# Optimization experiments

Hardware: AMD Instinct MI355X
Metric: run time of the kernel (lower is better)

## Reference

```python
import jax, jax.numpy as jnp
import numpy as np

RULE_START = 85
N_RULE = 20
N_OUTPUT = 33
N_RNN = 1024
T, B = 256, 256
ALPHA = 0.2
SIGMA = 0.05


def setup_inputs() -> dict:
    key = jax.random.key(0)
    ks = jax.random.split(key, 9)
    x = jax.random.normal(ks[0], (T, B, RULE_START + N_RULE), dtype=jnp.float32)
    # torch.rand_like -> uniform [0,1), scaled by sigma_rec (precomputed for all steps)
    noise = jax.random.uniform(ks[1], (T, B, N_RNN), dtype=jnp.float32) * SIGMA
    s = 0.05  # small init scale to keep softplus in a sane range
    W_sens = jax.random.normal(ks[2], (N_RNN, RULE_START), dtype=jnp.float32) * s
    b_sens = jax.random.normal(ks[3], (N_RNN,), dtype=jnp.float32) * s
    W_rule = jax.random.normal(ks[4], (N_RNN, N_RULE), dtype=jnp.float32) * s
    W_rec = jax.random.normal(ks[5], (N_RNN, N_RNN), dtype=jnp.float32) * s
    b_rec = jax.random.normal(ks[6], (N_RNN,), dtype=jnp.float32) * s
    W_out = jax.random.normal(ks[7], (N_OUTPUT, N_RNN), dtype=jnp.float32) * s
    b_out = jax.random.normal(ks[8], (N_OUTPUT,), dtype=jnp.float32) * s
    return {"x": x, "noise": noise, "W_sens": W_sens, "b_sens": b_sens,
            "W_rule": W_rule, "W_rec": W_rec, "b_rec": b_rec,
            "W_out": W_out, "b_out": b_out}


def reference(x, noise, W_sens, b_sens, W_rule, W_rec, b_rec, W_out, b_out):
    # x: [T, B, rule_start + n_rule]
    sensory = x[:, :, :RULE_START]
    rule = x[:, :, RULE_START:]
    # input projections applied once for all timesteps: [T, B, H]
    rnn_inputs = (jnp.einsum('tbi,hi->tbh', sensory, W_sens) + b_sens
                  + jnp.einsum('tbr,hr->tbh', rule, W_rule))

    h0 = jnp.zeros_like(rnn_inputs[0])  # [B, H]

    def step(h, inp_nz):
        inp, nz = inp_nz
        out = jax.nn.softplus(inp + nz + h @ W_rec.T + b_rec)
        h = ALPHA * out + (1.0 - ALPHA) * h
        return h, h

    _, hidden_states = jax.lax.scan(step, h0, (rnn_inputs, noise))  # [T, B, H]
    return jnp.einsum('tbh,oh->tbo', hidden_states, W_out) + b_out
```

## Files before the change

### kernel.cpp

```cpp
#include <hip/hip_runtime.h>
#include <cstdint>
#include <cstddef>

#define TSTEPS 256
#define NB     256
#define NH     1024
#define NIN    105
#define NOUT   33
#define NGRP   8
#define NSL    16

using half8 = __attribute__((ext_vector_type(8))) _Float16;
using f32x4 = __attribute__((ext_vector_type(4))) float;


__global__ __launch_bounds__(256) void k_convert(
    const float* __restrict__ W_sens, const float* __restrict__ W_rule,
    const float* __restrict__ W_rec,  const float* __restrict__ W_out,
    _Float16* __restrict__ Wrecf, _Float16* __restrict__ Wcf,
    _Float16* __restrict__ Wof)
{
    int tid  = blockIdx.x * 256 + threadIdx.x;
    int lane = tid & 63;
    int orow = lane & 15;
    int col0 = (lane >> 4) * 8;
    if (tid < 64 * 32 * 64) {
        int kk = (tid >> 6) & 31, n = tid >> 11;
        int o = n * 16 + orow, k0 = kk * 32 + col0;
        const float* s = W_rec + (size_t)o * NH + k0;
        _Float16* d = Wrecf + (size_t)tid * 8;
        #pragma unroll
        for (int j = 0; j < 8; ++j) d[j] = (_Float16)s[j];
    } else if (tid < 64 * 32 * 64 + 64 * 4 * 64) {
        int t2 = tid - 64 * 32 * 64;
        int kk = (t2 >> 6) & 3, n = t2 >> 8;
        int o = n * 16 + orow, k0 = kk * 32 + col0;
        _Float16* d = Wcf + (size_t)t2 * 8;
        #pragma unroll
        for (int j = 0; j < 8; ++j) {
            int k = k0 + j;
            float v = 0.f;
            if (k < 85)       v = W_sens[o * 85 + k];
            else if (k < NIN) v = W_rule[o * 20 + (k - 85)];
            d[j] = (_Float16)v;
        }
    } else {
        int t3 = tid - (64 * 32 * 64 + 64 * 4 * 64);
        int kk = (t3 >> 6) & 31, n = t3 >> 11;
        int o = n * 16 + orow, k0 = kk * 32 + col0;
        _Float16* d = Wof + (size_t)t3 * 8;
        #pragma unroll
        for (int j = 0; j < 8; ++j)
            d[j] = (o < NOUT) ? (_Float16)W_out[(size_t)o * NH + k0 + j]
                              : (_Float16)0.f;
    }
}

__global__ __launch_bounds__(256) void k_init(uint32_t* __restrict__ hGw,
                                              uint32_t* __restrict__ flags)
{
    int tid = blockIdx.x * 256 + threadIdx.x;
    if (tid < 262144) hGw[tid] = 0u;
    if (tid < 256)    flags[tid] = 0u;
}

#define XS_STRIDE 136
__global__ __launch_bounds__(256) void k_ingemm(
    const float* __restrict__ x, float* __restrict__ pre,
    const float* __restrict__ b_sens, const float* __restrict__ b_rec,
    const _Float16* __restrict__ Wcf)
{
    __shared__ _Float16 xs[64 * XS_STRIDE];
    int tid = threadIdx.x;
    int bm  = blockIdx.x;
    int nc  = blockIdx.y;
    const float* xsrc = x + (size_t)bm * 64 * NIN;
    for (int idx = tid; idx < 64 * NIN; idx += 256) {
        int r = idx / NIN, c = idx - r * NIN;
        xs[r * XS_STRIDE + c] = (_Float16)xsrc[idx];
    }
    for (int idx = tid; idx < 64 * (XS_STRIDE - NIN); idx += 256) {
        int r = idx / (XS_STRIDE - NIN);
        int c = NIN + (idx - r * (XS_STRIDE - NIN));
        xs[r * XS_STRIDE + c] = (_Float16)0.f;
    }
    __syncthreads();

    int wave = tid >> 6, lane = tid & 63;
    int mrow = lane & 15, q = lane >> 4;
    f32x4 acc[16];
    #pragma unroll
    for (int nt = 0; nt < 16; ++nt) acc[nt] = (f32x4){0.f, 0.f, 0.f, 0.f};
    const half8* Wc8 = (const half8*)Wcf;

    #pragma unroll
    for (int kk = 0; kk < 4; ++kk) {
        half8 a = *(const half8*)&xs[(wave * 16 + mrow) * XS_STRIDE + kk * 32 + q * 8];
        #pragma unroll
        for (int nt = 0; nt < 16; ++nt) {
            int ng = nc * 16 + nt;
            half8 b = Wc8[(ng * 4 + kk) * 64 + lane];
            acc[nt] = __builtin_amdgcn_mfma_f32_16x16x32_f16(a, b, acc[nt], 0, 0, 0);
        }
    }
    #pragma unroll
    for (int nt = 0; nt < 16; ++nt) {
        int o = nc * 256 + nt * 16 + mrow;
        float bias = b_sens[o] + b_rec[o];
        #pragma unroll
        for (int r = 0; r < 4; ++r) {
            size_t R = (size_t)bm * 64 + wave * 16 + q * 4 + r;
            size_t ad = R * NH + o;
            pre[ad] = acc[nt][r] + bias + pre[ad];
        }
    }
}

__global__ __launch_bounds__(512, 1) void k_rnn(
    float* __restrict__ pre, const _Float16* __restrict__ Wrecf,
    _Float16* __restrict__ hG, int* __restrict__ arr, int* __restrict__ xcdArr)
{
    __shared__ _Float16 Wl[4 * 32 * 64 * 8];
    __shared__ float red[8][64][4];
    __shared__ int sFast;

    const int tid  = threadIdx.x;
    const int blk  = blockIdx.x;
    const int g    = blk & 7, s = blk >> 3;
    const int wave = tid >> 6, lane = tid & 63;
    const int m    = wave & 1, kq = wave >> 1;
    const int mrow = lane & 15, q = lane >> 4;

    {
        const float4* src = (const float4*)(Wrecf + (size_t)(4 * s) * (32 * 64 * 8));
        float4* dst = (float4*)Wl;
        for (int i = tid; i < 8192; i += 512) dst[i] = src[i];
    }

    int xcd;
    asm volatile("s_getreg_b32 %0, hwreg(20, 0, 4)" : "=s"(xcd));
    if (tid == 0)
        __hip_atomic_store(&xcdArr[blk], xcd + 1, __ATOMIC_RELEASE,
                           __HIP_MEMORY_SCOPE_AGENT);
    if (wave == 0) {
        int idx = g + (lane & 15) * 8;
        int v = 0;
        for (int it = 0; it < (1 << 22); ++it) {
            v = __hip_atomic_load(&xcdArr[idx], __ATOMIC_ACQUIRE,
                                  __HIP_MEMORY_SCOPE_AGENT);
            if (__all(v >= 1)) break;
            __builtin_amdgcn_s_sleep(8);
        }
        if (lane == 0) sFast = __all(v == xcd + 1) ? 1 : 0;
    }
    __syncthreads();
    const bool fast = (sFast != 0);

    float hm[4][4];
    float pA[4][4];
    #pragma unroll
    for (int nt = 0; nt < 4; ++nt)
        #pragma unroll
        for (int r = 0; r < 4; ++r) hm[nt][r] = 0.f;
    if (kq == 0) {
        #pragma unroll
        for (int nt = 0; nt < 4; ++nt)
            #pragma unroll
            for (int r = 0; r < 4; ++r)
                pA[nt][r] = pre[(size_t)(g * 32 + m * 16 + q * 4 + r) * NH
                                + s * 64 + nt * 16 + mrow];
    }

    const size_t rowA = (size_t)(g * 32 + m * 16 + mrow);

    for (int t = 0; t < TSTEPS; ++t) {
        {
            int idx = g * 16 + (lane & 15);
            for (int it = 0; it < (1 << 22); ++it) {
                int v = __hip_atomic_load(&arr[idx], __ATOMIC_RELAXED,
                                          __HIP_MEMORY_SCOPE_AGENT);
                if (__all(v >= t)) break;
                __builtin_amdgcn_s_sleep(1);
            }
        }
        if (fast) {
            asm volatile("buffer_inv sc0" ::: "memory");
        } else {
            __builtin_amdgcn_fence(__ATOMIC_ACQUIRE, "agent");
        }

        const _Float16* hR = hG + (size_t)(t & 1) * (NGRP * 32 * 1024)
                                + rowA * 1024 + kq * 256 + q * 8;
        f32x4 acc[4];
        #pragma unroll
        for (int nt = 0; nt < 4; ++nt) acc[nt] = (f32x4){0.f, 0.f, 0.f, 0.f};
        #pragma unroll
        for (int kkl = 0; kkl < 8; ++kkl) {
            half8 a = *(const half8*)(hR + kkl * 32);
            #pragma unroll
            for (int nt = 0; nt < 4; ++nt) {
                half8 b = *(const half8*)&Wl[((nt * 32 + kq * 8 + kkl) * 64 + lane) * 8];
                acc[nt] = __builtin_amdgcn_mfma_f32_16x16x32_f16(a, b, acc[nt], 0, 0, 0);
            }
        }

        if (kq == 3) {
            #pragma unroll
            for (int nt = 0; nt < 4; ++nt)
                *(f32x4*)&red[m * 4 + nt][lane][0] = acc[nt];
        }
        __syncthreads();
        if (kq == 2) {
            #pragma unroll
            for (int nt = 0; nt < 4; ++nt) {
                f32x4 r = *(const f32x4*)&red[m * 4 + nt][lane][0];
                *(f32x4*)&red[m * 4 + nt][lane][0] = r + acc[nt];
            }
        }
        __syncthreads();
        if (kq == 1) {
            #pragma unroll
            for (int nt = 0; nt < 4; ++nt) {
                f32x4 r = *(const f32x4*)&red[m * 4 + nt][lane][0];
                *(f32x4*)&red[m * 4 + nt][lane][0] = r + acc[nt];
            }
        }
        __syncthreads();

        if (kq == 0) {
            _Float16* hW = hG + (size_t)((t + 1) & 1) * (NGRP * 32 * 1024);
            #pragma unroll
            for (int nt = 0; nt < 4; ++nt) {
                f32x4 rr = *(const f32x4*)&red[m * 4 + nt][lane][0];
                #pragma unroll
                for (int r = 0; r < 4; ++r) {
                    float v  = acc[nt][r] + rr[r] + pA[nt][r];
                    float sp = fmaxf(v, 0.f) + __logf(1.f + __expf(-fabsf(v)));
                    float hn = 0.2f * sp + 0.8f * hm[nt][r];
                    hm[nt][r] = hn;
                    int rl = m * 16 + q * 4 + r;
                    int cl = s * 64 + nt * 16 + mrow;
                    hW[(size_t)(g * 32 + rl) * 1024 + cl] = (_Float16)hn;
                    pre[((size_t)t * NB + g * 32 + rl) * NH + cl] = hn;
                }
            }
            if (t + 1 < TSTEPS) {
                #pragma unroll
                for (int nt = 0; nt < 4; ++nt)
                    #pragma unroll
                    for (int r = 0; r < 4; ++r)
                        pA[nt][r] = pre[((size_t)(t + 1) * NB + g * 32 + m * 16
                                         + q * 4 + r) * NH + s * 64 + nt * 16 + mrow];
            }
        }
        __syncthreads();

        if (!fast && tid == 0)
            __builtin_amdgcn_fence(__ATOMIC_RELEASE, "agent");
        if (tid == 0)
            __hip_atomic_store(&arr[g * 16 + s], t + 1, __ATOMIC_RELAXED,
                               __HIP_MEMORY_SCOPE_AGENT);
    }
}

__global__ __launch_bounds__(256) void k_out(
    const float* __restrict__ h, const _Float16* __restrict__ Wof,
    const float* __restrict__ b_out, float* __restrict__ y)
{
    int blk  = blockIdx.x;
    int wave = threadIdx.x >> 6, lane = threadIdx.x & 63;
    int mrow = lane & 15, q = lane >> 4;
    size_t row = (size_t)blk * 64 + wave * 16 + mrow;
    const half8* Wo8 = (const half8*)Wof;

    f32x4 acc[3];
    #pragma unroll
    for (int nt = 0; nt < 3; ++nt) acc[nt] = (f32x4){0.f, 0.f, 0.f, 0.f};

    #pragma unroll 4
    for (int kk = 0; kk < 32; ++kk) {
        const float4* hp = (const float4*)(h + row * NH + kk * 32 + q * 8);
        float4 f0 = hp[0], f1 = hp[1];
        half8 a = { (_Float16)f0.x, (_Float16)f0.y, (_Float16)f0.z, (_Float16)f0.w,
                    (_Float16)f1.x, (_Float16)f1.y, (_Float16)f1.z, (_Float16)f1.w };
        #pragma unroll
        for (int nt = 0; nt < 3; ++nt) {
            half8 b = Wo8[(nt * 32 + kk) * 64 + lane];
            acc[nt] = __builtin_amdgcn_mfma_f32_16x16x32_f16(a, b, acc[nt], 0, 0, 0);
        }
    }
    #pragma unroll
    for (int nt = 0; nt < 3; ++nt) {
        int o = nt * 16 + mrow;
        if (o < NOUT) {
            float bo = b_out[o];
            #pragma unroll
            for (int r = 0; r < 4; ++r) {
                size_t R = (size_t)blk * 64 + wave * 16 + q * 4 + r;
                y[R * NOUT + o] = acc[nt][r] + bo;
            }
        }
    }
}

extern "C" void kernel_launch(void* const* d_in, const int* in_sizes, int n_in,
                              void* d_out, int out_size, void* d_ws, size_t ws_size,
                              hipStream_t stream) {
    const float* x      = (const float*)d_in[0];
    float*       noise  = (float*)d_in[1];
    const float* W_sens = (const float*)d_in[2];
    const float* b_sens = (const float*)d_in[3];
    const float* W_rule = (const float*)d_in[4];
    const float* W_rec  = (const float*)d_in[5];
    const float* b_rec  = (const float*)d_in[6];
    const float* W_out  = (const float*)d_in[7];
    const float* b_out  = (const float*)d_in[8];
    float*       y      = (float*)d_out;

    _Float16* wsp   = (_Float16*)d_ws;
    _Float16* Wrecf = wsp;
    _Float16* Wcf   = Wrecf + 1048576;
    _Float16* Wof   = Wcf   + 131072;
    _Float16* hG    = Wof   + 49152;
    int*      arr   = (int*)(hG + 524288);
    int*      xcdArr= arr + 128;

    k_convert<<<dim3(600), dim3(256), 0, stream>>>(W_sens, W_rule, W_rec, W_out,
                                                   Wrecf, Wcf, Wof);
    k_init<<<dim3(1024), dim3(256), 0, stream>>>((uint32_t*)hG, (uint32_t*)arr);
    k_ingemm<<<dim3(1024, 4), dim3(256), 0, stream>>>(x, noise, b_sens, b_rec, Wcf);
    k_rnn<<<dim3(128), dim3(512), 0, stream>>>(noise, Wrecf, hG, arr, xcdArr);
    k_out<<<dim3(1024), dim3(256), 0, stream>>>(noise, Wof, b_out, y);
}
```

Measured before the change: 1.789 ms.

## Fuse input projection into recurrent kernel and store fp16 hidden history

```diff
diff --git a/kernel.cpp b/kernel.cpp
--- a/kernel.cpp
+++ b/kernel.cpp
@@ -7,8 +7,6 @@
 #define NH     1024
 #define NIN    105
 #define NOUT   33
-#define NGRP   8
-#define NSL    16
 
 using half8 = __attribute__((ext_vector_type(8))) _Float16;
 using f32x4 = __attribute__((ext_vector_type(4))) float;
@@ -56,72 +54,47 @@
     }
 }
 
-__global__ __launch_bounds__(256) void k_init(uint32_t* __restrict__ hGw,
-                                              uint32_t* __restrict__ flags)
-{
-    int tid = blockIdx.x * 256 + threadIdx.x;
-    if (tid < 262144) hGw[tid] = 0u;
-    if (tid < 256)    flags[tid] = 0u;
-}
-
-#define XS_STRIDE 136
-__global__ __launch_bounds__(256) void k_ingemm(
-    const float* __restrict__ x, float* __restrict__ pre,
+__global__ __launch_bounds__(256) void k_init(int* __restrict__ flags)
+{
+    if (threadIdx.x < 256) flags[threadIdx.x] = 0;
+}
+
+__device__ __forceinline__ void in_gemm(
+    const float* __restrict__ x, int tstep, int g, int m, int mrow, int q,
+    const half8 wcb[4][4], const float nzf[4][4], const float bias[4],
+    f32x4 pA[4])
+{
+    const float* xrow = x + ((size_t)tstep * NB + g * 32 + m * 16 + mrow) * NIN;
+    half8 af[4];
+    #pragma unroll
+    for (int kk = 0; kk < 4; ++kk) {
+        #pragma unroll
+        for (int j = 0; j < 8; ++j) {
+            int c = kk * 32 + q * 8 + j;
+            float v = (c < NIN) ? xrow[c] : 0.f;
+            af[kk][j] = (_Float16)v;
+        }
+    }
+    #pragma unroll
+    for (int nt = 0; nt < 4; ++nt) {
+        f32x4 c = { nzf[nt][0] + bias[nt], nzf[nt][1] + bias[nt],
+                    nzf[nt][2] + bias[nt], nzf[nt][3] + bias[nt] };
+        #pragma unroll
+        for (int kk = 0; kk < 4; ++kk)
+            c = __builtin_amdgcn_mfma_f32_16x16x32_f16(af[kk], wcb[nt][kk], c,
+                                                       0, 0, 0);
+        pA[nt] = c;
+    }
+}
+
+__global__ __launch_bounds__(512, 1) void k_rnn(
+    const float* __restrict__ x, float* __restrict__ noise,
     const float* __restrict__ b_sens, const float* __restrict__ b_rec,
-    const _Float16* __restrict__ Wcf)
-{
-    __shared__ _Float16 xs[64 * XS_STRIDE];
-    int tid = threadIdx.x;
-    int bm  = blockIdx.x;
-    int nc  = blockIdx.y;
-    const float* xsrc = x + (size_t)bm * 64 * NIN;
-    for (int idx = tid; idx < 64 * NIN; idx += 256) {
-        int r = idx / NIN, c = idx - r * NIN;
-        xs[r * XS_STRIDE + c] = (_Float16)xsrc[idx];
-    }
-    for (int idx = tid; idx < 64 * (XS_STRIDE - NIN); idx += 256) {
-        int r = idx / (XS_STRIDE - NIN);
-        int c = NIN + (idx - r * (XS_STRIDE - NIN));
-        xs[r * XS_STRIDE + c] = (_Float16)0.f;
-    }
-    __syncthreads();
-
-    int wave = tid >> 6, lane = tid & 63;
-    int mrow = lane & 15, q = lane >> 4;
-    f32x4 acc[16];
-    #pragma unroll
-    for (int nt = 0; nt < 16; ++nt) acc[nt] = (f32x4){0.f, 0.f, 0.f, 0.f};
-    const half8* Wc8 = (const half8*)Wcf;
-
-    #pragma unroll
-    for (int kk = 0; kk < 4; ++kk) {
-        half8 a = *(const half8*)&xs[(wave * 16 + mrow) * XS_STRIDE + kk * 32 + q * 8];
-        #pragma unroll
-        for (int nt = 0; nt < 16; ++nt) {
-            int ng = nc * 16 + nt;
-            half8 b = Wc8[(ng * 4 + kk) * 64 + lane];
-            acc[nt] = __builtin_amdgcn_mfma_f32_16x16x32_f16(a, b, acc[nt], 0, 0, 0);
-        }
-    }
-    #pragma unroll
-    for (int nt = 0; nt < 16; ++nt) {
-        int o = nc * 256 + nt * 16 + mrow;
-        float bias = b_sens[o] + b_rec[o];
-        #pragma unroll
-        for (int r = 0; r < 4; ++r) {
-            size_t R = (size_t)bm * 64 + wave * 16 + q * 4 + r;
-            size_t ad = R * NH + o;
-            pre[ad] = acc[nt][r] + bias + pre[ad];
-        }
-    }
-}
-
-__global__ __launch_bounds__(512, 1) void k_rnn(
-    float* __restrict__ pre, const _Float16* __restrict__ Wrecf,
-    _Float16* __restrict__ hG, int* __restrict__ arr, int* __restrict__ xcdArr)
+    const _Float16* __restrict__ Wrecf, const _Float16* __restrict__ Wcf,
+    int* __restrict__ arr, int* __restrict__ xcdArr)
 {
     __shared__ _Float16 Wl[4 * 32 * 64 * 8];
-    __shared__ float red[8][64][4];
+    __shared__ float red[3][8][64][4];
     __shared__ int sFast;
 
     const int tid  = threadIdx.x;
@@ -130,6 +103,9 @@
     const int wave = tid >> 6, lane = tid & 63;
     const int m    = wave & 1, kq = wave >> 1;
     const int mrow = lane & 15, q = lane >> 4;
+    const half8* Wc8 = (const half8*)Wcf;
+    _Float16* hist = (_Float16*)noise;
+    volatile int* varr = (volatile int*)arr;
 
     {
         const float4* src = (const float4*)(Wrecf + (size_t)(4 * s) * (32 * 64 * 8));
@@ -157,120 +133,139 @@
     const bool fast = (sFast != 0);
 
     float hm[4][4];
-    float pA[4][4];
+    f32x4 pA[4];
+    float nzf[4][4];
+    float bias[4];
+    half8 wcb[4][4];
     #pragma unroll
     for (int nt = 0; nt < 4; ++nt)
         #pragma unroll
         for (int r = 0; r < 4; ++r) hm[nt][r] = 0.f;
+
     if (kq == 0) {
         #pragma unroll
-        for (int nt = 0; nt < 4; ++nt)
+        for (int nt = 0; nt < 4; ++nt) {
+            int o = s * 64 + nt * 16 + mrow;
+            bias[nt] = b_sens[o] + b_rec[o];
+            #pragma unroll
+            for (int kk = 0; kk < 4; ++kk)
+                wcb[nt][kk] = Wc8[((4 * s + nt) * 4 + kk) * 64 + lane];
             #pragma unroll
             for (int r = 0; r < 4; ++r)
-                pA[nt][r] = pre[(size_t)(g * 32 + m * 16 + q * 4 + r) * NH
-                                + s * 64 + nt * 16 + mrow];
-    }
-
-    const size_t rowA = (size_t)(g * 32 + m * 16 + mrow);
+                nzf[nt][r] = noise[(size_t)(g * 32 + m * 16 + q * 4 + r) * NH
+                                   + s * 64 + nt * 16 + mrow];
+        }
+    }
+    __syncthreads();
+    if (tid == 0) {
+        if (fast) varr[g * 16 + s] = 1;
+        else __hip_atomic_store(&arr[g * 16 + s], 1, __ATOMIC_RELAXED,
+                                __HIP_MEMORY_SCOPE_AGENT);
+    }
+    if (kq == 0)
+        in_gemm(x, 0, g, m, mrow, q, wcb, nzf, bias, pA);
 
     for (int t = 0; t < TSTEPS; ++t) {
-        {
+        if (kq == 0 && t + 1 < TSTEPS) {
+            #pragma unroll
+            for (int nt = 0; nt < 4; ++nt)
+                #pragma unroll
+                for (int r = 0; r < 4; ++r)
+                    nzf[nt][r] = noise[((size_t)(t + 1) * NB + g * 32 + m * 16
+                                        + q * 4 + r) * NH
+                                       + s * 64 + nt * 16 + mrow];
+        }
+        if (wave == 0) {
             int idx = g * 16 + (lane & 15);
-            for (int it = 0; it < (1 << 22); ++it) {
-                int v = __hip_atomic_load(&arr[idx], __ATOMIC_RELAXED,
-                                          __HIP_MEMORY_SCOPE_AGENT);
-                if (__all(v >= t)) break;
-                __builtin_amdgcn_s_sleep(1);
-            }
-        }
-        if (fast) {
-            asm volatile("buffer_inv sc0" ::: "memory");
-        } else {
-            __builtin_amdgcn_fence(__ATOMIC_ACQUIRE, "agent");
-        }
-
-        const _Float16* hR = hG + (size_t)(t & 1) * (NGRP * 32 * 1024)
-                                + rowA * 1024 + kq * 256 + q * 8;
+            if (fast) {
+                for (int it = 0; it < (1 << 22); ++it) {
+                    asm volatile("buffer_inv sc0" ::: "memory");
+                    int v = varr[idx];
+                    if (__all(v >= t + 1)) break;
+                    __builtin_amdgcn_s_sleep(1);
+                }
+            } else {
+                for (int it = 0; it < (1 << 22); ++it) {
+                    int v = __hip_atomic_load(&arr[idx], __ATOMIC_RELAXED,
+                                              __HIP_MEMORY_SCOPE_AGENT);
+                    if (__all(v >= t + 1)) break;
+                    __builtin_amdgcn_s_sleep(1);
+                }
+            }
+        }
+        asm volatile("s_barrier" ::: "memory");
+        if (!fast) __builtin_amdgcn_fence(__ATOMIC_ACQUIRE, "agent");
+
         f32x4 acc[4];
         #pragma unroll
         for (int nt = 0; nt < 4; ++nt) acc[nt] = (f32x4){0.f, 0.f, 0.f, 0.f};
-        #pragma unroll
-        for (int kkl = 0; kkl < 8; ++kkl) {
-            half8 a = *(const half8*)(hR + kkl * 32);
+        if (t > 0) {
+            const _Float16* hR = hist + (size_t)(t - 1) * 524288
+                                      + (size_t)g * 65536
+                                      + (size_t)(m * 16 + mrow) * 1024
+                                      + kq * 256 + q * 8;
+            #pragma unroll
+            for (int kkl = 0; kkl < 8; ++kkl) {
+                half8 a = *(const half8*)(hR + kkl * 32);
+                #pragma unroll
+                for (int nt = 0; nt < 4; ++nt) {
+                    half8 b = *(const half8*)&Wl[((nt * 32 + kq * 8 + kkl) * 64
+                                                  + lane) * 8];
+                    acc[nt] = __builtin_amdgcn_mfma_f32_16x16x32_f16(a, b,
+                                                                acc[nt], 0, 0, 0);
+                }
+            }
+        }
+        if (kq != 0) {
+            #pragma unroll
+            for (int nt = 0; nt < 4; ++nt)
+                *(f32x4*)&red[kq - 1][m * 4 + nt][lane][0] = acc[nt];
+        }
+        asm volatile("s_waitcnt lgkmcnt(0)\n\ts_barrier" ::: "memory");
+
+        if (kq == 0) {
+            const size_t hb = (size_t)t * 524288 + (size_t)g * 65536;
             #pragma unroll
             for (int nt = 0; nt < 4; ++nt) {
-                half8 b = *(const half8*)&Wl[((nt * 32 + kq * 8 + kkl) * 64 + lane) * 8];
-                acc[nt] = __builtin_amdgcn_mfma_f32_16x16x32_f16(a, b, acc[nt], 0, 0, 0);
-            }
-        }
-
-        if (kq == 3) {
-            #pragma unroll
-            for (int nt = 0; nt < 4; ++nt)
-                *(f32x4*)&red[m * 4 + nt][lane][0] = acc[nt];
-        }
-        __syncthreads();
-        if (kq == 2) {
-            #pragma unroll
-            for (int nt = 0; nt < 4; ++nt) {
-                f32x4 r = *(const f32x4*)&red[m * 4 + nt][lane][0];
-                *(f32x4*)&red[m * 4 + nt][lane][0] = r + acc[nt];
-            }
-        }
-        __syncthreads();
-        if (kq == 1) {
-            #pragma unroll
-            for (int nt = 0; nt < 4; ++nt) {
-                f32x4 r = *(const f32x4*)&red[m * 4 + nt][lane][0];
-                *(f32x4*)&red[m * 4 + nt][lane][0] = r + acc[nt];
-            }
-        }
-        __syncthreads();
-
-        if (kq == 0) {
-            _Float16* hW = hG + (size_t)((t + 1) & 1) * (NGRP * 32 * 1024);
-            #pragma unroll
-            for (int nt = 0; nt < 4; ++nt) {
-                f32x4 rr = *(const f32x4*)&red[m * 4 + nt][lane][0];
+                f32x4 r0 = *(const f32x4*)&red[0][m * 4 + nt][lane][0];
+                f32x4 r1 = *(const f32x4*)&red[1][m * 4 + nt][lane][0];
+                f32x4 r2 = *(const f32x4*)&red[2][m * 4 + nt][lane][0];
                 #pragma unroll
                 for (int r = 0; r < 4; ++r) {
-                    float v  = acc[nt][r] + rr[r] + pA[nt][r];
+                    float v  = acc[nt][r] + r0[r] + r1[r] + r2[r] + pA[nt][r];
                     float sp = fmaxf(v, 0.f) + __logf(1.f + __expf(-fabsf(v)));
                     float hn = 0.2f * sp + 0.8f * hm[nt][r];
                     hm[nt][r] = hn;
-                    int rl = m * 16 + q * 4 + r;
-                    int cl = s * 64 + nt * 16 + mrow;
-                    hW[(size_t)(g * 32 + rl) * 1024 + cl] = (_Float16)hn;
-                    pre[((size_t)t * NB + g * 32 + rl) * NH + cl] = hn;
+                    hist[hb + (size_t)(m * 16 + q * 4 + r) * 1024
+                            + s * 64 + nt * 16 + mrow] = (_Float16)hn;
                 }
             }
-            if (t + 1 < TSTEPS) {
-                #pragma unroll
-                for (int nt = 0; nt < 4; ++nt)
-                    #pragma unroll
-                    for (int r = 0; r < 4; ++r)
-                        pA[nt][r] = pre[((size_t)(t + 1) * NB + g * 32 + m * 16
-                                         + q * 4 + r) * NH + s * 64 + nt * 16 + mrow];
-            }
-        }
-        __syncthreads();
-
-        if (!fast && tid == 0)
-            __builtin_amdgcn_fence(__ATOMIC_RELEASE, "agent");
-        if (tid == 0)
-            __hip_atomic_store(&arr[g * 16 + s], t + 1, __ATOMIC_RELAXED,
-                               __HIP_MEMORY_SCOPE_AGENT);
+        }
+        asm volatile("s_waitcnt vmcnt(0) lgkmcnt(0)\n\ts_barrier" ::: "memory");
+        if (tid == 0) {
+            if (fast) varr[g * 16 + s] = t + 2;
+            else {
+                __builtin_amdgcn_fence(__ATOMIC_RELEASE, "agent");
+                __hip_atomic_store(&arr[g * 16 + s], t + 2, __ATOMIC_RELAXED,
+                                   __HIP_MEMORY_SCOPE_AGENT);
+            }
+        }
+        if (kq == 0 && t + 1 < TSTEPS)
+            in_gemm(x, t + 1, g, m, mrow, q, wcb, nzf, bias, pA);
     }
 }
 
 __global__ __launch_bounds__(256) void k_out(
-    const float* __restrict__ h, const _Float16* __restrict__ Wof,
+    const _Float16* __restrict__ h16, const _Float16* __restrict__ Wof,
     const float* __restrict__ b_out, float* __restrict__ y)
 {
     int blk  = blockIdx.x;
     int wave = threadIdx.x >> 6, lane = threadIdx.x & 63;
     int mrow = lane & 15, q = lane >> 4;
-    size_t row = (size_t)blk * 64 + wave * 16 + mrow;
+    int t  = blk >> 2;
+    int b  = (blk & 3) * 64 + wave * 16 + mrow;
+    size_t hb = (size_t)t * 524288 + (size_t)(b >> 5) * 65536
+              + (size_t)(b & 31) * 1024;
     const half8* Wo8 = (const half8*)Wof;
 
     f32x4 acc[3];
@@ -279,14 +274,12 @@
 
     #pragma unroll 4
     for (int kk = 0; kk < 32; ++kk) {
-        const float4* hp = (const float4*)(h + row * NH + kk * 32 + q * 8);
-        float4 f0 = hp[0], f1 = hp[1];
-        half8 a = { (_Float16)f0.x, (_Float16)f0.y, (_Float16)f0.z, (_Float16)f0.w,
-                    (_Float16)f1.x, (_Float16)f1.y, (_Float16)f1.z, (_Float16)f1.w };
+        half8 a = *(const half8*)(h16 + hb + kk * 32 + q * 8);
         #pragma unroll
         for (int nt = 0; nt < 3; ++nt) {
-            half8 b = Wo8[(nt * 32 + kk) * 64 + lane];
-            acc[nt] = __builtin_amdgcn_mfma_f32_16x16x32_f16(a, b, acc[nt], 0, 0, 0);
+            half8 bb = Wo8[(nt * 32 + kk) * 64 + lane];
+            acc[nt] = __builtin_amdgcn_mfma_f32_16x16x32_f16(a, bb, acc[nt],
+                                                             0, 0, 0);
         }
     }
     #pragma unroll
@@ -321,14 +314,14 @@
     _Float16* Wrecf = wsp;
     _Float16* Wcf   = Wrecf + 1048576;
     _Float16* Wof   = Wcf   + 131072;
-    _Float16* hG    = Wof   + 49152;
-    int*      arr   = (int*)(hG + 524288);
+    int*      arr   = (int*)(Wof + 49152);
     int*      xcdArr= arr + 128;
 
     k_convert<<<dim3(600), dim3(256), 0, stream>>>(W_sens, W_rule, W_rec, W_out,
                                                    Wrecf, Wcf, Wof);
-    k_init<<<dim3(1024), dim3(256), 0, stream>>>((uint32_t*)hG, (uint32_t*)arr);
-    k_ingemm<<<dim3(1024, 4), dim3(256), 0, stream>>>(x, noise, b_sens, b_rec, Wcf);
-    k_rnn<<<dim3(128), dim3(512), 0, stream>>>(noise, Wrecf, hG, arr, xcdArr);
-    k_out<<<dim3(1024), dim3(256), 0, stream>>>(noise, Wof, b_out, y);
-}
+    k_init<<<dim3(1), dim3(256), 0, stream>>>(arr);
+    k_rnn<<<dim3(128), dim3(512), 0, stream>>>(x, noise, b_sens, b_rec,
+                                               Wrecf, Wcf, arr, xcdArr);
+    k_out<<<dim3(1024), dim3(256), 0, stream>>>((const _Float16*)noise, Wof,
+                                                b_out, y);
+}
```

Measured after the change: 1.698 ms. 5.1% less time.
